# Kernel tuning notes

Hardware: AMD Instinct MI355X
Metric: run time of the kernel (lower is better)

## Reference

```python
import jax, jax.numpy as jnp
import numpy as np
from jax import lax

# 4D convolution: XLA's general conv supports 4 spatial dims directly.
# dim numbers: N C + 4 spatial (H1 W1 H2 W2)
_DN = ('NCHWDT', 'OIHWDT', 'NCHWDT')


def conv4d(x, w, b):
    # x: [B, Cin, H1, W1, H2, W2]; w: [Cout, Cin, 3,3,3,3]; b: [Cout]
    y = lax.conv_general_dilated(x, w, window_strides=(1, 1, 1, 1),
                                 padding=[(1, 1)] * 4,
                                 dimension_numbers=_DN)
    return y + b.reshape(1, -1, 1, 1, 1, 1)


def setup_inputs() -> dict:
    key = jax.random.key(0)
    ks = jax.random.split(key, 7)
    B, S = 2, 30
    x = jax.random.normal(ks[0], (B, 1, S, S, S, S), dtype=jnp.float32)
    # Conv4d weights, fan-in scaled (kernel 3^4 = 81)
    w1 = jax.random.normal(ks[1], (10, 1, 3, 3, 3, 3), dtype=jnp.float32) * (1.0 / np.sqrt(1 * 81))
    b1 = jax.random.normal(ks[2], (10,), dtype=jnp.float32) * 0.01
    w2 = jax.random.normal(ks[3], (10, 10, 3, 3, 3, 3), dtype=jnp.float32) * (1.0 / np.sqrt(10 * 81))
    b2 = jax.random.normal(ks[4], (10,), dtype=jnp.float32) * 0.01
    w3 = jax.random.normal(ks[5], (1, 10, 3, 3, 3, 3), dtype=jnp.float32) * (1.0 / np.sqrt(10 * 81))
    b3 = jax.random.normal(ks[6], (1,), dtype=jnp.float32) * 0.01
    return {"x": x, "w1": w1, "b1": b1, "w2": w2, "b2": b2, "w3": w3, "b3": b3}


def reference(x, w1, b1, w2, b2, w3, b3):
    def net(t):
        for w, b in ((w1, b1), (w2, b2), (w3, b3)):
            t = jax.nn.relu(conv4d(t, w, b))
        return t

    # symmetric mode: f(x) + permute(f(permute(x)))
    perm = (0, 1, 4, 5, 2, 3)
    return net(x) + jnp.transpose(net(jnp.transpose(x, perm)), perm)
```

## Files before the change

kernel.cpp:

```cpp
#include <hip/hip_runtime.h>


static constexpr int S  = 30;
static constexpr long S4 = 810000;
static constexpr size_t PLANE = 32768;
static constexpr size_t YBYTES = (size_t)1800 * PLANE;

typedef __bf16 bf16x8 __attribute__((ext_vector_type(8)));
typedef float  f32x16 __attribute__((ext_vector_type(16)));
typedef unsigned int  u32;
typedef unsigned short u16;

static __device__ __forceinline__ u16 f2bf(float f) {
    u32 u = __builtin_bit_cast(u32, f);
    return (u16)((u + 0x7fffu + ((u >> 16) & 1u)) >> 16);
}

__global__ __launch_bounds__(256) void fragprep_k(u32* __restrict__ ft,
    const float* __restrict__ w1, const float* __restrict__ w2,
    const float* __restrict__ w3)
{
    const int gid = blockIdx.x * 256 + threadIdx.x;
    if (gid >= 6 * 27 * 64 + 2 * 3 * 64) return;
    const int lane = gid & 63;
    const int n = lane & 31, hl = lane >> 5;
    u16 us[8];
#pragma unroll
    for (int j = 0; j < 8; ++j) us[j] = 0;

    if (gid < 6 * 27 * 64) {
        int r = gid >> 6;
        const int k3 = r % 3; r /= 3;
        const int k12 = r % 9; const int set = r / 9;
        const int layer = set >> 1, swap = set & 1;
        const int k1 = k12 / 3, k2 = k12 % 3;
        if (n < 30) {
            const int k4 = (n < 10) ? 0 : ((n < 20) ? 1 : 2);
            const int co = n - 10 * k4;
            const int i1 = swap ? k3 : k1, i2 = swap ? k4 : k2;
            const int i3 = swap ? k1 : k3, i4 = swap ? k2 : k4;
            const int widx = ((i1 * 3 + i2) * 3 + i3) * 3 + i4;
#pragma unroll
            for (int j = 0; j < 8; ++j) {
                const int k = hl * 8 + j;
                float wv = 0.f;
                if (layer == 0) { if (k == 0) wv = w1[co * 81 + widx]; }
                else if (layer == 1) { if (k < 10) wv = w2[(co * 10 + k) * 81 + widx]; }
                else { if (k < 10 && co == 0) wv = w3[k * 81 + widx]; }
                us[j] = f2bf(wv);
            }
        }
    } else {
        const int idx = gid - 6 * 27 * 64;
        int r = idx >> 6;
        const int k3 = r % 3, swap = r / 3;
        if (n < 30) {
            const int k4 = (n < 10) ? 0 : ((n < 20) ? 1 : 2);
            const int co = n - 10 * k4;
#pragma unroll
            for (int j = 0; j < 8; ++j) {
                const int k12 = hl * 8 + j;
                if (k12 < 9) {
                    const int k1 = k12 / 3, k2 = k12 % 3;
                    const int i1 = swap ? k3 : k1, i2 = swap ? k4 : k2;
                    const int i3 = swap ? k1 : k3, i4 = swap ? k2 : k4;
                    const int widx = ((i1 * 3 + i2) * 3 + i3) * 3 + i4;
                    us[j] = f2bf(w1[co * 81 + widx]);
                }
            }
        }
    }
    u32* o = ft + (size_t)gid * 4;
    o[0] = (u32)us[0] | ((u32)us[1] << 16);
    o[1] = (u32)us[2] | ((u32)us[3] << 16);
    o[2] = (u32)us[4] | ((u32)us[5] << 16);
    o[3] = (u32)us[6] | ((u32)us[7] << 16);
}

__global__ __launch_bounds__(128) void zerok(u16* __restrict__ y1, u16* __restrict__ y2)
{
    const int pb = blockIdx.x, tid = threadIdx.x;
    if (tid >= 124) return;
    int hp, tp;
    if (tid < 32)      { hp = 0;        tp = tid; }
    else if (tid < 64) { hp = 31;       tp = tid - 32; }
    else if (tid < 94) { hp = tid - 63; tp = 0; }
    else               { hp = tid - 93; tp = 31; }
    const size_t off = (size_t)pb * PLANE + hp * 1024 + tp * 32;
    const uint4 z = make_uint4(0, 0, 0, 0);
    *(uint4*)((char*)y1 + off)      = z;
    *(uint4*)((char*)y1 + off + 16) = z;
    *(uint4*)((char*)y2 + off)      = z;
    *(uint4*)((char*)y2 + off + 16) = z;
}

__global__ __launch_bounds__(256, 4) void conv0_k(
    const float* __restrict__ x, const uint4* __restrict__ bt,
    const float* __restrict__ bias, void* __restrict__ outp)
{
    __shared__ float E[4][1056];
    const int wgid = blockIdx.x + S * blockIdx.y + 900 * blockIdx.z;
    const int id2  = (wgid & 7) * 450 + (wgid >> 3);
    const int half = id2 & 1;
    int sp = id2 >> 1;
    const int w1i = sp % S; sp /= S;
    const int h1  = sp % S;
    const int b   = sp / S;

    const int tid = threadIdx.x;
    const int lane = tid & 63, wv = tid >> 6;
    const int m = lane & 31, hl = lane >> 5;
    const int rbase = half * 15 + wv * 4;

    uint4 Bs[3];
#pragma unroll
    for (int ss = 0; ss < 3; ++ss) Bs[ss] = bt[ss * 64 + lane];

    int gof[9]; int gokm = 0;
#pragma unroll
    for (int k12 = 0; k12 < 9; ++k12) {
        const int g1 = h1 + k12 / 3 - 1, g2 = w1i + k12 % 3 - 1;
        gof[k12] = 0;
        if (g1 >= 0 && g1 < S && g2 >= 0 && g2 < S) {
            gof[k12] = (g1 * S + g2) * 900; gokm |= 1 << k12;
        }
    }
    const float* xb = x + (size_t)b * S4;

    uint4 F[6];
#pragma unroll
    for (int f = 0; f < 6; ++f) {
        const int hp = rbase + f;
        const bool rk = (hp >= 1 && hp <= 30 && m >= 1 && m <= 30);
        const int ro = (hp - 1) * 30 + (m - 1);
        u16 av[8];
#pragma unroll
        for (int j = 0; j < 8; ++j) av[j] = 0;
        if (hl == 0) {
#pragma unroll
            for (int j = 0; j < 8; ++j) {
                float v = 0.f;
                if (rk && ((gokm >> j) & 1)) v = xb[gof[j] + ro];
                av[j] = f2bf(v);
            }
        } else {
            float v = 0.f;
            if (rk && ((gokm >> 8) & 1)) v = xb[gof[8] + ro];
            av[0] = f2bf(v);
        }
        F[f] = make_uint4((u32)av[0] | ((u32)av[1] << 16),
                          (u32)av[2] | ((u32)av[3] << 16),
                          (u32)av[4] | ((u32)av[5] << 16),
                          (u32)av[6] | ((u32)av[7] << 16));
    }

    f32x16 acc[4];
#pragma unroll
    for (int r = 0; r < 4; ++r)
#pragma unroll
        for (int e = 0; e < 16; ++e) acc[r][e] = 0.f;
#pragma unroll
    for (int ss = 0; ss < 3; ++ss)
#pragma unroll
        for (int r = 0; r < 4; ++r)
            acc[r] = __builtin_amdgcn_mfma_f32_32x32x16_bf16(
                __builtin_bit_cast(bf16x8, F[r + ss]),
                __builtin_bit_cast(bf16x8, Bs[ss]), acc[r], 0, 0, 0);

    float* Ew = E[wv];
    for (int r = 0; r < 4; ++r) {
        if (wv == 3 && r == 3) continue;
#pragma unroll
        for (int gq = 0; gq < 4; ++gq)
#pragma unroll
            for (int r4 = 0; r4 < 4; ++r4)
                Ew[m * 33 + 4 * hl + 8 * gq + r4] = acc[r][gq * 4 + r4];

        const int h2 = rbase + r;
        char* pl = (char*)outp + ((size_t)b * 900 + h1 * S + w1i) * PLANE
                   + (size_t)(h2 + 1) * 1024;
        const int t = lane >> 1, h8 = lane & 1;
        if (t < 30) {
            u32 wo[4];
#pragma unroll
            for (int p = 0; p < 4; ++p) {
                const int c0 = 8 * h8 + 2 * p, c1 = c0 + 1;
                float v0 = 0.f, v1 = 0.f;
                if (c0 < 10)
                    v0 = fmaxf(Ew[c0 * 33 + t] + Ew[(10 + c0) * 33 + t + 1]
                             + Ew[(20 + c0) * 33 + t + 2] + bias[c0], 0.f);
                if (c1 < 10)
                    v1 = fmaxf(Ew[c1 * 33 + t] + Ew[(10 + c1) * 33 + t + 1]
                             + Ew[(20 + c1) * 33 + t + 2] + bias[c1], 0.f);
                wo[p] = (u32)f2bf(v0) | ((u32)f2bf(v1) << 16);
            }
            *(uint4*)(pl + (t + 1) * 32 + h8 * 16) =
                make_uint4(wo[0], wo[1], wo[2], wo[3]);
        }
    }
}

template<int LAYER, bool ACCUM>
__global__ __launch_bounds__(256, 2) void conv_k(
    const void* __restrict__ inp, const u32* __restrict__ ftab,
    const float* __restrict__ bias, void* __restrict__ outp)
{
    __shared__ float E[4][1056];
    __shared__ uint4 BT[1728];

    const int tid = threadIdx.x;
    {
        const uint4* g = (const uint4*)ftab;
#pragma unroll
        for (int j = 0; j < 7; ++j) {
            const int idx = j * 256 + tid;
            if (idx < 1728) BT[idx] = g[idx];
        }
    }
    __syncthreads();

    const int wgid = blockIdx.x + S * blockIdx.y + 900 * blockIdx.z;
    const int id2  = (wgid & 7) * 450 + (wgid >> 3);
    const int half = id2 & 1;
    int sp = id2 >> 1;
    const int w1i = sp % S; sp /= S;
    const int h1  = sp % S;
    const int b   = sp / S;

    const int lane = tid & 63, wv = tid >> 6;
    const int m = lane & 31, hl = lane >> 5;
    const int rbase = half * 15 + wv * 4;

    int rofs[6];
#pragma unroll
    for (int f = 0; f < 6; ++f) {
        int rr = rbase + f; if (rr > 31) rr = 31;
        rofs[f] = rr * 1024;
    }

    int kl[9], nk = 0;
#pragma unroll
    for (int k12 = 0; k12 < 9; ++k12) {
        const int g1 = h1 + k12 / 3 - 1, g2 = w1i + k12 % 3 - 1;
        if (g1 >= 0 && g1 < S && g2 >= 0 && g2 < S)
            kl[nk++] = (g1 * S + g2) | (k12 << 10);
    }

    f32x16 acc[4];
#pragma unroll
    for (int r = 0; r < 4; ++r)
#pragma unroll
        for (int e = 0; e < 16; ++e) acc[r][e] = 0.f;

    auto loadA = [&](uint4* Fd, int g) {
        const char* P = (const char*)inp + ((size_t)b * 900 + g) * PLANE
                        + m * 32 + hl * 16;
#pragma unroll
        for (int f = 0; f < 6; ++f)
            Fd[f] = *(const uint4*)(P + rofs[f]);
    };

    uint4 B0[3];
    {
        const int k0 = kl[0] >> 10;
#pragma unroll
        for (int f = 0; f < 3; ++f) B0[f] = BT[(k0 * 3 + f) * 64 + lane];
    }
    uint4 F[6];
    loadA(F, kl[0] & 1023);

    for (int ki = 0; ki + 1 < nk; ++ki) {
        const int gn = kl[ki + 1] & 1023, kn = kl[ki + 1] >> 10;
        uint4 FN[6];
        loadA(FN, gn);
        uint4 BN[3];
#pragma unroll
        for (int f = 0; f < 3; ++f) BN[f] = BT[(kn * 3 + f) * 64 + lane];

#pragma unroll
        for (int ss = 0; ss < 3; ++ss)
#pragma unroll
            for (int r = 0; r < 4; ++r)
                acc[r] = __builtin_amdgcn_mfma_f32_32x32x16_bf16(
                    __builtin_bit_cast(bf16x8, F[r + ss]),
                    __builtin_bit_cast(bf16x8, B0[ss]), acc[r], 0, 0, 0);

#pragma unroll
        for (int f = 0; f < 6; ++f) F[f] = FN[f];
#pragma unroll
        for (int f = 0; f < 3; ++f) B0[f] = BN[f];
    }
#pragma unroll
    for (int ss = 0; ss < 3; ++ss)
#pragma unroll
        for (int r = 0; r < 4; ++r)
            acc[r] = __builtin_amdgcn_mfma_f32_32x32x16_bf16(
                __builtin_bit_cast(bf16x8, F[r + ss]),
                __builtin_bit_cast(bf16x8, B0[ss]), acc[r], 0, 0, 0);

    float* Ew = E[wv];
    for (int r = 0; r < 4; ++r) {
        if (wv == 3 && r == 3) continue;
#pragma unroll
        for (int gq = 0; gq < 4; ++gq)
#pragma unroll
            for (int r4 = 0; r4 < 4; ++r4)
                Ew[m * 33 + 4 * hl + 8 * gq + r4] = acc[r][gq * 4 + r4];

        const int h2 = rbase + r;
        if (LAYER <= 1) {
            char* pl = (char*)outp + ((size_t)b * 900 + h1 * S + w1i) * PLANE
                       + (size_t)(h2 + 1) * 1024;
            const int t = lane >> 1, h8 = lane & 1;
            if (t < 30) {
                u32 wo[4];
#pragma unroll
                for (int p = 0; p < 4; ++p) {
                    const int c0 = 8 * h8 + 2 * p, c1 = c0 + 1;
                    float v0 = 0.f, v1 = 0.f;
                    if (c0 < 10)
                        v0 = fmaxf(Ew[c0 * 33 + t] + Ew[(10 + c0) * 33 + t + 1]
                                 + Ew[(20 + c0) * 33 + t + 2] + bias[c0], 0.f);
                    if (c1 < 10)
                        v1 = fmaxf(Ew[c1 * 33 + t] + Ew[(10 + c1) * 33 + t + 1]
                                 + Ew[(20 + c1) * 33 + t + 2] + bias[c1], 0.f);
                    wo[p] = (u32)f2bf(v0) | ((u32)f2bf(v1) << 16);
                }
                *(uint4*)(pl + (t + 1) * 32 + h8 * 16) =
                    make_uint4(wo[0], wo[1], wo[2], wo[3]);
            }
        } else {
            if (lane < 30) {
                const int t = lane;
                float v = Ew[t] + Ew[330 + t + 1] + Ew[660 + t + 2] + bias[0];
                v = fmaxf(v, 0.f);
                float* o = (float*)outp + (size_t)b * S4
                           + (size_t)(h1 * S + w1i) * 900 + h2 * 30 + t;
                if (ACCUM) *o += v; else *o = v;
            }
        }
    }
}

extern "C" void kernel_launch(void* const* d_in, const int* in_sizes, int n_in,
                              void* d_out, int out_size, void* d_ws, size_t ws_size,
                              hipStream_t stream)
{
    const float* x   = (const float*)d_in[0];
    const float* w1p = (const float*)d_in[1];
    const float* b1p = (const float*)d_in[2];
    const float* w2p = (const float*)d_in[3];
    const float* b2p = (const float*)d_in[4];
    const float* w3p = (const float*)d_in[5];
    const float* b3p = (const float*)d_in[6];
    float* out = (float*)d_out;

    u32* ft = (u32*)d_ws;
    const uint4* ftL0 = (const uint4*)d_ws + 6 * 27 * 64;
    u16* y1 = (u16*)((char*)d_ws + 172032);
    u16* y2 = (u16*)((char*)y1 + YBYTES);

    fragprep_k<<<42, 256, 0, stream>>>(ft, w1p, w2p, w3p);
    zerok<<<1800, 128, 0, stream>>>(y1, y2);

    dim3 grid(S, S, 4), blk(256);
    for (int br = 0; br < 2; ++br) {
        const u32* f2 = ft + (size_t)(2 + br) * 27 * 64 * 4;
        const u32* f3 = ft + (size_t)(4 + br) * 27 * 64 * 4;
        conv0_k<<<grid, blk, 0, stream>>>(x, ftL0 + br * 192, b1p, (void*)y1);
        conv_k<1, false><<<grid, blk, 0, stream>>>(y1, f2, b2p, (void*)y2);
        if (br == 0)
            conv_k<2, false><<<grid, blk, 0, stream>>>(y2, f3, b3p, (void*)out);
        else
            conv_k<2, true><<<grid, blk, 0, stream>>>(y2, f3, b3p, (void*)out);
    }
}
```

Before: 387.1 us.

## Drop software prefetch in conv main loop and raise occupancy to 4 blocks

Removes the register double-buffering of A fragments and B weights across kernel taps. Each tap now loads directly with constant offsets from a single base pointer, and the row clamp is replaced by one precomputed offset. The launch bound moves from 2 to 4 blocks per CU so more waves can hide memory latency in place of per-wave prefetch. The cost is that each wave now waits on its loads before its MFMAs, and the tighter register budget could cause spills; shared memory use may also cap how many blocks actually fit.

```diff
diff --git a/kernel.cpp b/kernel.cpp
--- a/kernel.cpp
+++ b/kernel.cpp
@@ -201,7 +201,7 @@
 }
 
 template<int LAYER, bool ACCUM>
-__global__ __launch_bounds__(256, 2) void conv_k(
+__global__ __launch_bounds__(256, 4) void conv_k(
     const void* __restrict__ inp, const u32* __restrict__ ftab,
     const float* __restrict__ bias, void* __restrict__ outp)
 {
@@ -230,13 +230,7 @@
     const int lane = tid & 63, wv = tid >> 6;
     const int m = lane & 31, hl = lane >> 5;
     const int rbase = half * 15 + wv * 4;
-
-    int rofs[6];
-#pragma unroll
-    for (int f = 0; f < 6; ++f) {
-        int rr = rbase + f; if (rr > 31) rr = 31;
-        rofs[f] = rr * 1024;
-    }
+    const int off5 = (rbase == 27) ? 4096 : 5120;
 
     int kl[9], nk = 0;
 #pragma unroll
@@ -252,30 +246,22 @@
 #pragma unroll
         for (int e = 0; e < 16; ++e) acc[r][e] = 0.f;
 
-    auto loadA = [&](uint4* Fd, int g) {
-        const char* P = (const char*)inp + ((size_t)b * 900 + g) * PLANE
-                        + m * 32 + hl * 16;
-#pragma unroll
-        for (int f = 0; f < 6; ++f)
-            Fd[f] = *(const uint4*)(P + rofs[f]);
-    };
-
-    uint4 B0[3];
-    {
-        const int k0 = kl[0] >> 10;
-#pragma unroll
-        for (int f = 0; f < 3; ++f) B0[f] = BT[(k0 * 3 + f) * 64 + lane];
-    }
-    uint4 F[6];
-    loadA(F, kl[0] & 1023);
-
-    for (int ki = 0; ki + 1 < nk; ++ki) {
-        const int gn = kl[ki + 1] & 1023, kn = kl[ki + 1] >> 10;
-        uint4 FN[6];
-        loadA(FN, gn);
-        uint4 BN[3];
-#pragma unroll
-        for (int f = 0; f < 3; ++f) BN[f] = BT[(kn * 3 + f) * 64 + lane];
+    const char* Pb = (const char*)inp + (size_t)b * 900 * PLANE
+                     + (size_t)rbase * 1024 + m * 32 + hl * 16;
+
+    for (int ki = 0; ki < nk; ++ki) {
+        const int g = kl[ki] & 1023, kk = kl[ki] >> 10;
+        const char* P = Pb + (size_t)g * PLANE;
+        uint4 F[6];
+        F[0] = *(const uint4*)(P);
+        F[1] = *(const uint4*)(P + 1024);
+        F[2] = *(const uint4*)(P + 2048);
+        F[3] = *(const uint4*)(P + 3072);
+        F[4] = *(const uint4*)(P + 4096);
+        F[5] = *(const uint4*)(P + off5);
+        uint4 B0[3];
+#pragma unroll
+        for (int f = 0; f < 3; ++f) B0[f] = BT[(kk * 3 + f) * 64 + lane];
 
 #pragma unroll
         for (int ss = 0; ss < 3; ++ss)
@@ -284,19 +270,7 @@
                 acc[r] = __builtin_amdgcn_mfma_f32_32x32x16_bf16(
                     __builtin_bit_cast(bf16x8, F[r + ss]),
                     __builtin_bit_cast(bf16x8, B0[ss]), acc[r], 0, 0, 0);
-
-#pragma unroll
-        for (int f = 0; f < 6; ++f) F[f] = FN[f];
-#pragma unroll
-        for (int f = 0; f < 3; ++f) B0[f] = BN[f];
-    }
-#pragma unroll
-    for (int ss = 0; ss < 3; ++ss)
-#pragma unroll
-        for (int r = 0; r < 4; ++r)
-            acc[r] = __builtin_amdgcn_mfma_f32_32x32x16_bf16(
-                __builtin_bit_cast(bf16x8, F[r + ss]),
-                __builtin_bit_cast(bf16x8, B0[ss]), acc[r], 0, 0, 0);
+    }
 
     float* Ew = E[wv];
     for (int r = 0; r < 4; ++r) {
```

After: 450.2 us. 1.16x slower.

## Merge prep kernels and fuse layer-3 of branch 0 with layer-1 of branch 1

Applied to the files above, without the earlier changes.

Combines weight-fragment prep and border zeroing into one launch. Fuses the independent branch-0 final conv with the branch-1 first conv into a single grid of 8 z-slices to cut launches and fill tails. Adds s_setprio around MFMA blocks to favour matrix issue. The conv0 path now runs with the heavier conv kernel's shared memory and launch bounds, which may reduce its occupancy.

```diff
diff --git a/kernel.cpp b/kernel.cpp
--- a/kernel.cpp
+++ b/kernel.cpp
@@ -16,12 +16,28 @@
     return (u16)((u + 0x7fffu + ((u >> 16) & 1u)) >> 16);
 }
 
-__global__ __launch_bounds__(256) void fragprep_k(u32* __restrict__ ft,
+__global__ __launch_bounds__(256) void prep_k(u32* __restrict__ ft,
     const float* __restrict__ w1, const float* __restrict__ w2,
-    const float* __restrict__ w3)
-{
-    const int gid = blockIdx.x * 256 + threadIdx.x;
-    if (gid >= 6 * 27 * 64 + 2 * 3 * 64) return;
+    const float* __restrict__ w3, u16* __restrict__ y1, u16* __restrict__ y2)
+{
+    const int tid = threadIdx.x;
+    if (blockIdx.x >= 42) {
+        const int pb = blockIdx.x - 42;
+        if (tid >= 124) return;
+        int hp, tp;
+        if (tid < 32)      { hp = 0;        tp = tid; }
+        else if (tid < 64) { hp = 31;       tp = tid - 32; }
+        else if (tid < 94) { hp = tid - 63; tp = 0; }
+        else               { hp = tid - 93; tp = 31; }
+        const size_t off = (size_t)pb * PLANE + hp * 1024 + tp * 32;
+        const uint4 z = make_uint4(0, 0, 0, 0);
+        *(uint4*)((char*)y1 + off)      = z;
+        *(uint4*)((char*)y1 + off + 16) = z;
+        *(uint4*)((char*)y2 + off)      = z;
+        *(uint4*)((char*)y2 + off + 16) = z;
+        return;
+    }
+    const int gid = blockIdx.x * 256 + tid;
     const int lane = gid & 63;
     const int n = lane & 31, hl = lane >> 5;
     u16 us[8];
@@ -77,29 +93,11 @@
     o[3] = (u32)us[6] | ((u32)us[7] << 16);
 }
 
-__global__ __launch_bounds__(128) void zerok(u16* __restrict__ y1, u16* __restrict__ y2)
-{
-    const int pb = blockIdx.x, tid = threadIdx.x;
-    if (tid >= 124) return;
-    int hp, tp;
-    if (tid < 32)      { hp = 0;        tp = tid; }
-    else if (tid < 64) { hp = 31;       tp = tid - 32; }
-    else if (tid < 94) { hp = tid - 63; tp = 0; }
-    else               { hp = tid - 93; tp = 31; }
-    const size_t off = (size_t)pb * PLANE + hp * 1024 + tp * 32;
-    const uint4 z = make_uint4(0, 0, 0, 0);
-    *(uint4*)((char*)y1 + off)      = z;
-    *(uint4*)((char*)y1 + off + 16) = z;
-    *(uint4*)((char*)y2 + off)      = z;
-    *(uint4*)((char*)y2 + off + 16) = z;
-}
-
-__global__ __launch_bounds__(256, 4) void conv0_k(
-    const float* __restrict__ x, const uint4* __restrict__ bt,
-    const float* __restrict__ bias, void* __restrict__ outp)
-{
-    __shared__ float E[4][1056];
-    const int wgid = blockIdx.x + S * blockIdx.y + 900 * blockIdx.z;
+static __device__ __forceinline__ void conv0_body(
+    float (*E)[1056], const float* __restrict__ x, const uint4* __restrict__ bt,
+    const float* __restrict__ bias, void* __restrict__ outp, int zq)
+{
+    const int wgid = blockIdx.x + S * blockIdx.y + 900 * zq;
     const int id2  = (wgid & 7) * 450 + (wgid >> 3);
     const int half = id2 & 1;
     int sp = id2 >> 1;
@@ -159,6 +157,7 @@
     for (int r = 0; r < 4; ++r)
 #pragma unroll
         for (int e = 0; e < 16; ++e) acc[r][e] = 0.f;
+    __builtin_amdgcn_s_setprio(1);
 #pragma unroll
     for (int ss = 0; ss < 3; ++ss)
 #pragma unroll
@@ -166,6 +165,7 @@
             acc[r] = __builtin_amdgcn_mfma_f32_32x32x16_bf16(
                 __builtin_bit_cast(bf16x8, F[r + ss]),
                 __builtin_bit_cast(bf16x8, Bs[ss]), acc[r], 0, 0, 0);
+    __builtin_amdgcn_s_setprio(0);
 
     float* Ew = E[wv];
     for (int r = 0; r < 4; ++r) {
@@ -200,14 +200,20 @@
     }
 }
 
+__global__ __launch_bounds__(256, 4) void conv0_k(
+    const float* __restrict__ x, const uint4* __restrict__ bt,
+    const float* __restrict__ bias, void* __restrict__ outp)
+{
+    __shared__ float E[4][1056];
+    conv0_body(E, x, bt, bias, outp, blockIdx.z);
+}
+
 template<int LAYER, bool ACCUM>
-__global__ __launch_bounds__(256, 2) void conv_k(
+static __device__ __forceinline__ void conv_body(
+    float (*E)[1056], uint4* BT,
     const void* __restrict__ inp, const u32* __restrict__ ftab,
-    const float* __restrict__ bias, void* __restrict__ outp)
-{
-    __shared__ float E[4][1056];
-    __shared__ uint4 BT[1728];
-
+    const float* __restrict__ bias, void* __restrict__ outp, int zq)
+{
     const int tid = threadIdx.x;
     {
         const uint4* g = (const uint4*)ftab;
@@ -219,7 +225,7 @@
     }
     __syncthreads();
 
-    const int wgid = blockIdx.x + S * blockIdx.y + 900 * blockIdx.z;
+    const int wgid = blockIdx.x + S * blockIdx.y + 900 * zq;
     const int id2  = (wgid & 7) * 450 + (wgid >> 3);
     const int half = id2 & 1;
     int sp = id2 >> 1;
@@ -277,6 +283,7 @@
 #pragma unroll
         for (int f = 0; f < 3; ++f) BN[f] = BT[(kn * 3 + f) * 64 + lane];
 
+        __builtin_amdgcn_s_setprio(1);
 #pragma unroll
         for (int ss = 0; ss < 3; ++ss)
 #pragma unroll
@@ -284,12 +291,14 @@
                 acc[r] = __builtin_amdgcn_mfma_f32_32x32x16_bf16(
                     __builtin_bit_cast(bf16x8, F[r + ss]),
                     __builtin_bit_cast(bf16x8, B0[ss]), acc[r], 0, 0, 0);
+        __builtin_amdgcn_s_setprio(0);
 
 #pragma unroll
         for (int f = 0; f < 6; ++f) F[f] = FN[f];
 #pragma unroll
         for (int f = 0; f < 3; ++f) B0[f] = BN[f];
     }
+    __builtin_amdgcn_s_setprio(1);
 #pragma unroll
     for (int ss = 0; ss < 3; ++ss)
 #pragma unroll
@@ -297,6 +306,7 @@
             acc[r] = __builtin_amdgcn_mfma_f32_32x32x16_bf16(
                 __builtin_bit_cast(bf16x8, F[r + ss]),
                 __builtin_bit_cast(bf16x8, B0[ss]), acc[r], 0, 0, 0);
+    __builtin_amdgcn_s_setprio(0);
 
     float* Ew = E[wv];
     for (int r = 0; r < 4; ++r) {
@@ -342,6 +352,31 @@
     }
 }
 
+template<int LAYER, bool ACCUM>
+__global__ __launch_bounds__(256, 2) void conv_k(
+    const void* __restrict__ inp, const u32* __restrict__ ftab,
+    const float* __restrict__ bias, void* __restrict__ outp)
+{
+    __shared__ float E[4][1056];
+    __shared__ uint4 BT[1728];
+    conv_body<LAYER, ACCUM>(E, BT, inp, ftab, bias, outp, blockIdx.z);
+}
+
+__global__ __launch_bounds__(256, 2) void conv20_k(
+    const void* __restrict__ y2, const u32* __restrict__ ft2,
+    const float* __restrict__ b3, float* __restrict__ out,
+    const float* __restrict__ x, const uint4* __restrict__ bt0,
+    const float* __restrict__ b1, void* __restrict__ y1)
+{
+    __shared__ float E[4][1056];
+    __shared__ uint4 BT[1728];
+    const int bz = blockIdx.z;
+    if (bz < 4)
+        conv_body<2, false>(E, BT, y2, ft2, b3, (void*)out, bz);
+    else
+        conv0_body(E, x, bt0, b1, y1, bz - 4);
+}
+
 extern "C" void kernel_launch(void* const* d_in, const int* in_sizes, int n_in,
                               void* d_out, int out_size, void* d_ws, size_t ws_size,
                               hipStream_t stream)
@@ -360,18 +395,18 @@
     u16* y1 = (u16*)((char*)d_ws + 172032);
     u16* y2 = (u16*)((char*)y1 + YBYTES);
 
-    fragprep_k<<<42, 256, 0, stream>>>(ft, w1p, w2p, w3p);
-    zerok<<<1800, 128, 0, stream>>>(y1, y2);
-
-    dim3 grid(S, S, 4), blk(256);
-    for (int br = 0; br < 2; ++br) {
-        const u32* f2 = ft + (size_t)(2 + br) * 27 * 64 * 4;
-        const u32* f3 = ft + (size_t)(4 + br) * 27 * 64 * 4;
-        conv0_k<<<grid, blk, 0, stream>>>(x, ftL0 + br * 192, b1p, (void*)y1);
-        conv_k<1, false><<<grid, blk, 0, stream>>>(y1, f2, b2p, (void*)y2);
-        if (br == 0)
-            conv_k<2, false><<<grid, blk, 0, stream>>>(y2, f3, b3p, (void*)out);
-        else
-            conv_k<2, true><<<grid, blk, 0, stream>>>(y2, f3, b3p, (void*)out);
-    }
-}
+    prep_k<<<1842, 256, 0, stream>>>(ft, w1p, w2p, w3p, y1, y2);
+
+    const u32* f2b0 = ft + (size_t)2 * 27 * 64 * 4;
+    const u32* f2b1 = ft + (size_t)3 * 27 * 64 * 4;
+    const u32* f3b0 = ft + (size_t)4 * 27 * 64 * 4;
+    const u32* f3b1 = ft + (size_t)5 * 27 * 64 * 4;
+
+    dim3 g4(S, S, 4), g8(S, S, 8), blk(256);
+    conv0_k<<<g4, blk, 0, stream>>>(x, ftL0 + 0 * 192, b1p, (void*)y1);
+    conv_k<1, false><<<g4, blk, 0, stream>>>(y1, f2b0, b2p, (void*)y2);
+    conv20_k<<<g8, blk, 0, stream>>>(y2, f3b0, b3p, out,
+                                     x, ftL0 + 1 * 192, b1p, (void*)y1);
+    conv_k<1, false><<<g4, blk, 0, stream>>>(y1, f2b1, b2p, (void*)y2);
+    conv_k<2, true><<<g4, blk, 0, stream>>>(y2, f3b1, b3p, (void*)out);
+}
```

Result: slower. 457.9 us (+18.3%).
